# Optimization experiments

Measured on AMD Instinct MI355X. Metric: run time of the kernel, lower is better.

## Reference

```python
import jax, jax.numpy as jnp
import numpy as np

N_QUBITS = 12
N_LAYERS = 5
OUTPUT_DIM = 4
BATCH = 1024


def _apply_1q(state, U, q, n):
    # state: (B, 2^n) complex; U: (B, 2, 2) per-sample unitary on wire q
    B = state.shape[0]
    s = state.reshape(B, 2 ** q, 2, -1)
    s = jnp.einsum('bik,bakc->baic', U, s)
    return s.reshape(B, -1)


def _cnot(state, c, t, n):
    # CNOT with control wire c, target wire t (wire 0 = most significant bit)
    B = state.shape[0]
    s = state.reshape((B,) + (2,) * n)
    s0 = jax.lax.index_in_dim(s, 0, axis=1 + c, keepdims=True)
    s1 = jax.lax.index_in_dim(s, 1, axis=1 + c, keepdims=True)
    s1 = jnp.flip(s1, axis=1 + t)  # X on target where control = 1
    return jnp.concatenate([s0, s1], axis=1 + c).reshape(B, -1)


def _forward(x, input_weights, theta, output_weights):
    n, L, D = N_QUBITS, N_LAYERS, OUTPUT_DIM
    x = jnp.tanh(x)
    B = x.shape[0]
    # |0...0> initial state, batched
    state = jnp.zeros((B, 2 ** n), jnp.complex64).at[:, 0].set(1.0)
    for l in range(L):
        # data re-uploading: RX(input_weights[l,j] * x[:,j]) on every wire, every layer
        a = input_weights[l][None, :] * x          # (B, n) RX angles
        b = theta[l, :, 0]                          # (n,) RY angles
        c = theta[l, :, 1]                          # (n,) RZ angles
        ca = jnp.cos(a / 2).astype(jnp.complex64)
        sa = jnp.sin(a / 2).astype(jnp.complex64)
        Rx = jnp.stack([jnp.stack([ca, -1j * sa], -1),
                        jnp.stack([-1j * sa, ca], -1)], -2)  # (B, n, 2, 2)
        cb = jnp.cos(b / 2).astype(jnp.complex64)
        sb = jnp.sin(b / 2).astype(jnp.complex64)
        ec = jnp.exp(-1j * c.astype(jnp.complex64) / 2)      # e^{-i c/2}
        # M = RZ(c) @ RY(b), shared across the batch
        M = jnp.stack([jnp.stack([ec * cb, -ec * sb], -1),
                       jnp.stack([jnp.conj(ec) * sb, jnp.conj(ec) * cb], -1)], -2)  # (n,2,2)
        # fused single-qubit unitary U = RZ @ RY @ RX per (sample, wire)
        U = jnp.einsum('qik,bqkj->bqij', M, Rx)
        for q in range(n):
            state = _apply_1q(state, U[:, q], q, n)
        for i in range(n):
            state = _cnot(state, i, (i + 1) % n, n)
    # exact <Z_i> on the first D wires
    p = jnp.abs(state) ** 2  # (B, 2^n)
    zs = []
    for i in range(D):
        pr = p.reshape(B, 2 ** i, 2, -1)
        zs.append(pr[:, :, 0, :].sum((1, 2)) - pr[:, :, 1, :].sum((1, 2)))
    Q = jnp.stack(zs, axis=1)  # (B, D)
    return output_weights[None, :] * Q


def setup_inputs() -> dict:
    key = jax.random.key(0)
    k1, k2, k3, k4 = jax.random.split(key, 4)
    return {
        'x': jax.random.normal(k1, (BATCH, N_QUBITS), jnp.float32),
        'input_weights': jax.random.normal(k2, (N_LAYERS, N_QUBITS), jnp.float32),
        'theta': jax.random.normal(k3, (N_LAYERS, N_QUBITS, 2), jnp.float32),
        'output_weights': jax.random.normal(k4, (OUTPUT_DIM,), jnp.float32),
    }


def reference(x, input_weights, theta, output_weights):
    return _forward(x, input_weights, theta, output_weights)
```

## Files before the change

kernel.cpp:

```cpp
#include <hip/hip_runtime.h>

#define NQ 12
#define NL 5
#define TPB 256

__host__ __device__ constexpr int sfx12_(int x) {
    x ^= x >> 1; x ^= x >> 2; x ^= x >> 4; x ^= x >> 8;
    return x & 0xFFF;
}
__host__ __device__ constexpr int par_(int x) {
    int y = x; y ^= y >> 8; y ^= y >> 4; y ^= y >> 2; y ^= y >> 1;
    return y & 1;
}
__host__ __device__ constexpr int amp_addr(int i) {
    const int g = i >> 1;
    const int G = g ^ ((g >> 3) & 7);
    return (G << 4) | ((i & 1) << 3);
}
__host__ __device__ constexpr int scat_c(int m) {
    const int s = sfx12_(m << 8);
    return amp_addr(s ^ ((s & 1) << 11));
}
__host__ __device__ constexpr int bpat(int m) { return amp_addr(m << 4); }
__host__ __device__ constexpr int meas_h(int m) {
    const int d = sfx12_(m << 8) ^ (par_(m) << 11);
    return (d >> 8) & 15;
}

__device__ __forceinline__ void gate_pair(float2 &a, float2 &c,
        const float2 u00, const float2 u01, const float2 u10, const float2 u11) {
    float2 n0, n1;
    n0.x = fmaf(u00.x, a.x, fmaf(-u00.y, a.y, fmaf(u01.x, c.x, -u01.y * c.y)));
    n0.y = fmaf(u00.x, a.y, fmaf( u00.y, a.x, fmaf(u01.x, c.y,  u01.y * c.x)));
    n1.x = fmaf(u10.x, a.x, fmaf(-u10.y, a.y, fmaf(u11.x, c.x, -u11.y * c.y)));
    n1.y = fmaf(u10.x, a.y, fmaf( u10.y, a.x, fmaf(u11.x, c.y,  u11.y * c.x)));
    a = n0; c = n1;
}
template <int K>
__device__ __forceinline__ void apply_gate(float2 (&v)[16], const float2* __restrict__ Uq) {
    const float2 u00 = Uq[0], u01 = Uq[1], u10 = Uq[2], u11 = Uq[3];
#pragma unroll
    for (int h = 0; h < 8; ++h) {
        const int m0 = ((h >> K) << (K + 1)) | (h & ((1 << K) - 1));
        gate_pair(v[m0], v[m0 | (1 << K)], u00, u01, u10, u11);
    }
}

extern "C" __global__ void __launch_bounds__(TPB)
qnet_kernel(const float* __restrict__ x, const float* __restrict__ iw,
            const float* __restrict__ th, const float* __restrict__ ow,
            float* __restrict__ out) {
    __shared__ float2 st[4096];
    __shared__ __align__(16) float2 U[NL][NQ][4];
    __shared__ float wz[4][4];
    char* stb = (char*)st;

    const int b = blockIdx.x;
    const int tid = threadIdx.x;
    const int w = tid >> 6;

    if (tid < NL * NQ) {
        const int l = tid / NQ, q = tid % NQ;
        const float xv = tanhf(x[b * NQ + q]);
        const float a = iw[l * NQ + q] * xv;
        const float bt = th[(l * NQ + q) * 2 + 0];
        const float ct = th[(l * NQ + q) * 2 + 1];
        float sa, ca; sincosf(0.5f * a, &sa, &ca);
        float sb, cb; sincosf(0.5f * bt, &sb, &cb);
        float sc, cc; sincosf(0.5f * ct, &sc, &cc);
        const float M00r = cc * cb, M00i = -sc * cb;
        const float M01r = -cc * sb, M01i = sc * sb;
        const float M10r = cc * sb, M10i = sc * sb;
        const float M11r = cc * cb, M11i = sc * cb;
        U[l][q][0] = make_float2(fmaf(M00r, ca,  sa * M01i), fmaf(M00i, ca, -sa * M01r));
        U[l][q][1] = make_float2(fmaf(ca, M01r,  sa * M00i), fmaf(ca, M01i, -sa * M00r));
        U[l][q][2] = make_float2(fmaf(M10r, ca,  sa * M11i), fmaf(M10i, ca, -sa * M11r));
        U[l][q][3] = make_float2(fmaf(ca, M11r,  sa * M10i), fmaf(ca, M11i, -sa * M10r));
    }

    const int baseA = amp_addr(tid << 4);
    const int baseB = amp_addr(((tid >> 4) << 8) | (tid & 15));
    const int baseC = amp_addr(tid);
    const int pt = __popc(tid) & 1;
    const int baseS = amp_addr(sfx12_(tid) ^ (pt << 11));
    const int hT = pt << 3;

    __syncthreads();

    float2 v[16];
#pragma unroll 1
    for (int l = 0; l < NL; ++l) {
        if (l == 0) {
#pragma unroll
            for (int r = 0; r < 16; ++r) v[r] = make_float2(0.f, 0.f);
            if (tid == 0) v[0].x = 1.f;
        } else {
#pragma unroll
            for (int c = 0; c < 8; ++c) {
                const float4 f = *(const float4*)(stb + (baseA ^ (c << 4)));
                v[2 * c]     = make_float2(f.x, f.y);
                v[2 * c + 1] = make_float2(f.z, f.w);
            }
        }
        apply_gate<0>(v, U[l][11]);
        apply_gate<1>(v, U[l][10]);
        apply_gate<2>(v, U[l][9]);
        apply_gate<3>(v, U[l][8]);
#pragma unroll
        for (int c = 0; c < 8; ++c)
            *(float4*)(stb + (baseA ^ (c << 4))) =
                make_float4(v[2 * c].x, v[2 * c].y, v[2 * c + 1].x, v[2 * c + 1].y);
        __syncthreads();

#pragma unroll
        for (int m = 0; m < 16; ++m)
            v[m] = *(const float2*)(stb + (baseB ^ bpat(m)));
        apply_gate<0>(v, U[l][7]);
        apply_gate<1>(v, U[l][6]);
        apply_gate<2>(v, U[l][5]);
        apply_gate<3>(v, U[l][4]);
#pragma unroll
        for (int m = 0; m < 16; ++m)
            *(float2*)(stb + (baseB ^ bpat(m))) = v[m];
        __syncthreads();

#pragma unroll
        for (int m = 0; m < 16; ++m)
            v[m] = *(const float2*)(stb + baseC + (m << 11));
        apply_gate<0>(v, U[l][3]);
        apply_gate<1>(v, U[l][2]);
        apply_gate<2>(v, U[l][1]);
        apply_gate<3>(v, U[l][0]);

        if (l != NL - 1) {
            __syncthreads();
#pragma unroll
            for (int m = 0; m < 16; ++m)
                *(float2*)(stb + (baseS ^ scat_c(m))) = v[m];
            __syncthreads();
        }
    }

    float z0 = 0.f, z1 = 0.f, z2 = 0.f, z3 = 0.f;
#pragma unroll
    for (int m = 0; m < 16; ++m) {
        const float pr = fmaf(v[m].x, v[m].x, v[m].y * v[m].y);
        const int h = meas_h(m) ^ hT;
        z0 += (h & 8) ? -pr : pr;
        z1 += (h & 4) ? -pr : pr;
        z2 += (h & 2) ? -pr : pr;
        z3 += (h & 1) ? -pr : pr;
    }
#pragma unroll
    for (int off = 32; off > 0; off >>= 1) {
        z0 += __shfl_xor(z0, off);
        z1 += __shfl_xor(z1, off);
        z2 += __shfl_xor(z2, off);
        z3 += __shfl_xor(z3, off);
    }
    if ((tid & 63) == 0) {
        wz[w][0] = z0; wz[w][1] = z1; wz[w][2] = z2; wz[w][3] = z3;
    }
    __syncthreads();
    if (tid < 4) {
        const float z = wz[0][tid] + wz[1][tid] + wz[2][tid] + wz[3][tid];
        out[b * 4 + tid] = ow[tid] * z;
    }
}

extern "C" void kernel_launch(void* const* d_in, const int* in_sizes, int n_in,
                              void* d_out, int out_size, void* d_ws, size_t ws_size,
                              hipStream_t stream) {
    const float* x  = (const float*)d_in[0];
    const float* iw = (const float*)d_in[1];
    const float* th = (const float*)d_in[2];
    const float* ow = (const float*)d_in[3];
    float* out = (float*)d_out;
    const int batch = in_sizes[0] / NQ;
    hipLaunchKernelGGL(qnet_kernel, dim3(batch), dim3(TPB), 0, stream,
                       x, iw, th, ow, out);
}
```

Measured before the change: 50.34 us.

## Use packed-FP32 complex gate math, unroll layers, and measure from shared memory

Replaces the scalar FMA complex 2x2 gate with inline v_pk_mul/v_pk_fma packed FP32 instructions, roughly halving VALU instruction count per gate. It fully unrolls the layer loop and always performs the final CNOT scatter to shared memory, then computes <Z> from contiguous float4 reads instead of the permuted register-based measurement. It also adds a duplicated unitary-setup block with a strange '* 0.f' term, which is redundant work. The unroll may increase register pressure and code size, and the extra scatter and barriers add shared-memory traffic.

After: 49.18 us. 1.02x faster.

```diff
diff --git a/kernel.cpp b/kernel.cpp
--- a/kernel.cpp
+++ b/kernel.cpp
@@ -7,10 +7,6 @@
 __host__ __device__ constexpr int sfx12_(int x) {
     x ^= x >> 1; x ^= x >> 2; x ^= x >> 4; x ^= x >> 8;
     return x & 0xFFF;
-}
-__host__ __device__ constexpr int par_(int x) {
-    int y = x; y ^= y >> 8; y ^= y >> 4; y ^= y >> 2; y ^= y >> 1;
-    return y & 1;
 }
 __host__ __device__ constexpr int amp_addr(int i) {
     const int g = i >> 1;
@@ -22,27 +18,40 @@
     return amp_addr(s ^ ((s & 1) << 11));
 }
 __host__ __device__ constexpr int bpat(int m) { return amp_addr(m << 4); }
-__host__ __device__ constexpr int meas_h(int m) {
-    const int d = sfx12_(m << 8) ^ (par_(m) << 11);
-    return (d >> 8) & 15;
-}
-
-__device__ __forceinline__ void gate_pair(float2 &a, float2 &c,
-        const float2 u00, const float2 u01, const float2 u10, const float2 u11) {
-    float2 n0, n1;
-    n0.x = fmaf(u00.x, a.x, fmaf(-u00.y, a.y, fmaf(u01.x, c.x, -u01.y * c.y)));
-    n0.y = fmaf(u00.x, a.y, fmaf( u00.y, a.x, fmaf(u01.x, c.y,  u01.y * c.x)));
-    n1.x = fmaf(u10.x, a.x, fmaf(-u10.y, a.y, fmaf(u11.x, c.x, -u11.y * c.y)));
-    n1.y = fmaf(u10.x, a.y, fmaf( u10.y, a.x, fmaf(u11.x, c.y,  u11.y * c.x)));
-    a = n0; c = n1;
-}
+
+__device__ __forceinline__ float2 cmul_pk(float2 u, float2 un, float2 z) {
+    float2 d, t;
+    asm("v_pk_mul_f32 %1, %3, %4 op_sel:[0,1] op_sel_hi:[1,0]\n\t"
+        "v_pk_fma_f32 %0, %2, %4, %1 op_sel:[0,0,0] op_sel_hi:[0,1,1]"
+        : "=v"(d), "=&v"(t)
+        : "v"(u), "v"(un), "v"(z));
+    return d;
+}
+__device__ __forceinline__ float2 cfma_pk(float2 u, float2 un, float2 z, float2 c) {
+    float2 d, t;
+    asm("v_pk_fma_f32 %1, %3, %4, %5 op_sel:[0,1,0] op_sel_hi:[1,0,1]\n\t"
+        "v_pk_fma_f32 %0, %2, %4, %1 op_sel:[0,0,0] op_sel_hi:[0,1,1]"
+        : "=v"(d), "=&v"(t)
+        : "v"(u), "v"(un), "v"(z), "v"(c));
+    return d;
+}
+
 template <int K>
 __device__ __forceinline__ void apply_gate(float2 (&v)[16], const float2* __restrict__ Uq) {
     const float2 u00 = Uq[0], u01 = Uq[1], u10 = Uq[2], u11 = Uq[3];
+    const float2 u00n = make_float2(-u00.y, u00.y);
+    const float2 u01n = make_float2(-u01.y, u01.y);
+    const float2 u10n = make_float2(-u10.y, u10.y);
+    const float2 u11n = make_float2(-u11.y, u11.y);
 #pragma unroll
     for (int h = 0; h < 8; ++h) {
         const int m0 = ((h >> K) << (K + 1)) | (h & ((1 << K) - 1));
-        gate_pair(v[m0], v[m0 | (1 << K)], u00, u01, u10, u11);
+        const int m1 = m0 | (1 << K);
+        const float2 a = v[m0], c = v[m1];
+        const float2 n0 = cfma_pk(u00, u00n, a, cmul_pk(u01, u01n, c));
+        const float2 n1 = cfma_pk(u10, u10n, a, cmul_pk(u11, u11n, c));
+        v[m0] = n0;
+        v[m1] = n1;
     }
 }
 
@@ -59,6 +68,25 @@
     const int tid = threadIdx.x;
     const int w = tid >> 6;
 
+    if (tid < NL * NQ) {
+        const int l = tid / NQ, q = tid % NQ;
+        const float xv = tanhf(x[b * NQ + q]);
+        const float a = iw[l * NQ + q] * xv;
+        const float bt = th[(l * NQ + q) * 2 + 0];
+        const float ct = th[(l * NQ + q) * 2 + 1];
+        float sa, ca; sincosf(0.5f * a, &sa, &ca);
+        float sb, cb; sincosf(0.5f * bt, &sb, &cb);
+        float sc, cc; sincosf(0.5f * ct, &sc, &cc);
+        const float M00r = cc * cb, M00i = -sc * cb;
+        const float M01r = -cc * sb, M01i = sc * sb;
+        const float M10r = cc * sb, M10i = sc * sb;
+        const float M11r = cc * cb, M11i = sc * cb;
+        U[l][q][0] = make_float2(fmaf(M00r, ca,  sa * M01i), fmaf(M00i, ca, -sa * M01r));
+        U[l][q][1] = make_float2(fmaf(ca, M01r,  sa * M00i), fmaf(ca, M01i, -sa * M00r));
+        U[l][q][2] = make_float2(fmaf(M10r, ca,  sa * M11i), fmaf(M10i, ca, -sa * M11r));
+        U[l][q][3] = make_float2(fmaf(ca, M11r,  sa * M11i * 0.f + sa * M10i),
+                                 fmaf(ca, M11i, -sa * M10r));
+    }
     if (tid < NL * NQ) {
         const int l = tid / NQ, q = tid % NQ;
         const float xv = tanhf(x[b * NQ + q]);
@@ -83,12 +111,11 @@
     const int baseC = amp_addr(tid);
     const int pt = __popc(tid) & 1;
     const int baseS = amp_addr(sfx12_(tid) ^ (pt << 11));
-    const int hT = pt << 3;
 
     __syncthreads();
 
     float2 v[16];
-#pragma unroll 1
+#pragma unroll
     for (int l = 0; l < NL; ++l) {
         if (l == 0) {
 #pragma unroll
@@ -131,35 +158,32 @@
         apply_gate<1>(v, U[l][2]);
         apply_gate<2>(v, U[l][1]);
         apply_gate<3>(v, U[l][0]);
-
-        if (l != NL - 1) {
-            __syncthreads();
-#pragma unroll
-            for (int m = 0; m < 16; ++m)
-                *(float2*)(stb + (baseS ^ scat_c(m))) = v[m];
-            __syncthreads();
-        }
-    }
-
-    float z0 = 0.f, z1 = 0.f, z2 = 0.f, z3 = 0.f;
-#pragma unroll
-    for (int m = 0; m < 16; ++m) {
-        const float pr = fmaf(v[m].x, v[m].x, v[m].y * v[m].y);
-        const int h = meas_h(m) ^ hT;
-        z0 += (h & 8) ? -pr : pr;
-        z1 += (h & 4) ? -pr : pr;
-        z2 += (h & 2) ? -pr : pr;
-        z3 += (h & 1) ? -pr : pr;
-    }
+        __syncthreads();
+#pragma unroll
+        for (int m = 0; m < 16; ++m)
+            *(float2*)(stb + (baseS ^ scat_c(m))) = v[m];
+        __syncthreads();
+    }
+
+    float ps = 0.f;
+#pragma unroll
+    for (int c = 0; c < 8; ++c) {
+        const float4 f = *(const float4*)(stb + (baseA ^ (c << 4)));
+        ps = fmaf(f.x, f.x, fmaf(f.y, f.y, fmaf(f.z, f.z, fmaf(f.w, f.w, ps))));
+    }
+    float s0 = (tid & 128) ? -ps : ps;
+    float s1 = (tid & 64) ? -ps : ps;
+    float s2 = (tid & 32) ? -ps : ps;
+    float s3 = (tid & 16) ? -ps : ps;
 #pragma unroll
     for (int off = 32; off > 0; off >>= 1) {
-        z0 += __shfl_xor(z0, off);
-        z1 += __shfl_xor(z1, off);
-        z2 += __shfl_xor(z2, off);
-        z3 += __shfl_xor(z3, off);
+        s0 += __shfl_xor(s0, off);
+        s1 += __shfl_xor(s1, off);
+        s2 += __shfl_xor(s2, off);
+        s3 += __shfl_xor(s3, off);
     }
     if ((tid & 63) == 0) {
-        wz[w][0] = z0; wz[w][1] = z1; wz[w][2] = z2; wz[w][3] = z3;
+        wz[w][0] = s0; wz[w][1] = s1; wz[w][2] = s2; wz[w][3] = s3;
     }
     __syncthreads();
     if (tid < 4) {
```
